# Performance work log

Hardware: AMD Instinct MI355X
Metric: run time of the kernel (lower is better)

The kernel has to match this reference:

```python
import jax, jax.numpy as jnp
import numpy as np

NUM_HEADS = 16
HEAD_DIM = 64
ROT_DIM = HEAD_DIM // 2  # RotaryEmbedding(dim=head_dim/2) rotates first 32 dims only
THETA = 10000.0


def _rope(x):
    # x: [b, h, l, d]; interleaved (lucidrains) rotary on first ROT_DIM dims.
    L = x.shape[-2]
    inv_freq = 1.0 / (THETA ** (jnp.arange(0, ROT_DIM, 2, dtype=jnp.float32) / ROT_DIM))  # [ROT_DIM/2]
    ang = jnp.arange(L, dtype=jnp.float32)[:, None] * inv_freq[None, :]  # [l, ROT_DIM/2]
    ang = jnp.repeat(ang, 2, axis=-1)  # [l, ROT_DIM] (each freq repeated for the pair)
    cos, sin = jnp.cos(ang), jnp.sin(ang)
    x_rot, x_pass = x[..., :ROT_DIM], x[..., ROT_DIM:]
    x1 = x_rot[..., 0::2]
    x2 = x_rot[..., 1::2]
    rot_half = jnp.stack([-x2, x1], axis=-1).reshape(x_rot.shape)  # rotate_half, interleaved
    x_rot = x_rot * cos + rot_half * sin
    return jnp.concatenate([x_rot, x_pass], axis=-1)


def setup_inputs() -> dict:
    key = jax.random.key(0)
    ks = jax.random.split(key, 7)
    B, L, E = 2, 2048, 1024
    s = 1.0 / np.sqrt(E)
    return {
        "query": jax.random.normal(ks[0], (B, L, E), jnp.float32),
        "key": jax.random.normal(ks[1], (B, L, E), jnp.float32),
        "value": jax.random.normal(ks[2], (B, L, E), jnp.float32),
        "Wq": jax.random.normal(ks[3], (E, E), jnp.float32) * s,
        "Wk": jax.random.normal(ks[4], (E, E), jnp.float32) * s,
        "Wv": jax.random.normal(ks[5], (E, E), jnp.float32) * s,
        "Wo": jax.random.normal(ks[6], (E, E), jnp.float32) * s,
        "bo": jnp.zeros((E,), jnp.float32),
    }


def reference(query, key, value, Wq, Wk, Wv, Wo, bo):
    B, L, E = query.shape
    H, D = NUM_HEADS, HEAD_DIM
    scaling = D ** (-0.5)

    def split_heads(x):
        return x.reshape(B, L, H, D).transpose(0, 2, 1, 3)  # b h l d

    q = split_heads(query @ Wq.T)
    k = split_heads(key @ Wk.T)
    v = split_heads(value @ Wv.T)
    q = _rope(q)
    k = _rope(k)
    # NOTE: source divides by scaling (multiplies by sqrt(D)) -- faithful to original.
    attn_weight = jnp.einsum('bhid,bhjd->bhij', q, k) / scaling
    # NOTE: softmax over dim=-2 (query axis), as in the original code.
    attn_weight = jax.nn.softmax(attn_weight, axis=-2)
    attn = jnp.einsum('bhij,bhjd->bhid', attn_weight, v)
    attn = attn.transpose(0, 2, 1, 3).reshape(B, L, E)
    out = attn @ Wo.T + bo
    return out, attn_weight
```

## Files before the change

### kernel.cpp

```cpp
#include <hip/hip_runtime.h>
#include <cmath>

typedef __bf16 bf16;
typedef __attribute__((ext_vector_type(4))) __bf16 bf16x4;
typedef __attribute__((ext_vector_type(8))) __bf16 bf16x8;
typedef __attribute__((ext_vector_type(4))) float f32x4;

#define MFMA16(a, b, c) __builtin_amdgcn_mfma_f32_16x16x32_bf16((a), (b), (c), 0, 0, 0)
#define SETPRIO1 __builtin_amdgcn_s_setprio(1)
#define SETPRIO0 __builtin_amdgcn_s_setprio(0)
#define EXP2(x) __builtin_amdgcn_exp2f(x)
#define WAITV_BAR(N) asm volatile("s_waitcnt vmcnt(" #N ")\n\ts_barrier" ::: "memory")
#define WAITL_BAR    asm volatile("s_waitcnt lgkmcnt(0)\n\ts_barrier" ::: "memory")

#define LOG2E 1.4426950408889634f

static __device__ __forceinline__ void gload16(const bf16* g, bf16* l)
{
  __builtin_amdgcn_global_load_lds((const __attribute__((address_space(1))) void*)g,
                                   (__attribute__((address_space(3))) void*)l, 16, 0, 0);
}

static __device__ __forceinline__ void split4(const float4 v, bf16x4& h, bf16x4& l)
{
  h[0] = (bf16)v.x; l[0] = (bf16)(v.x - (float)h[0]);
  h[1] = (bf16)v.y; l[1] = (bf16)(v.y - (float)h[1]);
  h[2] = (bf16)v.z; l[2] = (bf16)(v.z - (float)h[2]);
  h[3] = (bf16)v.w; l[3] = (bf16)(v.w - (float)h[3]);
}

__global__ __launch_bounds__(256) void conv_kernel(
    const float* __restrict__ query, const float* __restrict__ key, const float* __restrict__ value,
    const float* __restrict__ Wq, const float* __restrict__ Wk, const float* __restrict__ Wv,
    const float* __restrict__ Wo,
    bf16* __restrict__ qh, bf16* __restrict__ ql, bf16* __restrict__ kh, bf16* __restrict__ kl,
    bf16* __restrict__ wqh, bf16* __restrict__ wql, bf16* __restrict__ wkh, bf16* __restrict__ wkl,
    bf16* __restrict__ vb, bf16* __restrict__ wvb, bf16* __restrict__ wob)
{
  const int i = blockIdx.x * 256 + threadIdx.x;
  const float* src;
  bf16 *dh, *dl;
  int e;
  if (i < 1048576)      { src = query; dh = qh; dl = ql; e = i; }
  else if (i < 2097152) { src = key;   dh = kh; dl = kl; e = i - 1048576; }
  else if (i < 3145728) { src = value; dh = vb; dl = nullptr; e = i - 2097152; }
  else {
    const int w = i - 3145728;
    const int which = w >> 18;
    e = w & 262143;
    src = (which == 0) ? Wq : (which == 1) ? Wk : (which == 2) ? Wv : Wo;
    dh  = (which == 0) ? wqh : (which == 1) ? wkh : (which == 2) ? wvb : wob;
    dl  = (which == 0) ? wql : (which == 1) ? wkl : nullptr;
  }
  const float4 v = ((const float4*)src)[e];
  bf16x4 h, l;
  split4(v, h, l);
  *(bf16x4*)(dh + (size_t)e * 4) = h;
  if (dl) *(bf16x4*)(dl + (size_t)e * 4) = l;
}

__global__ __launch_bounds__(256) void projqk_kernel(
    const bf16* __restrict__ qh, const bf16* __restrict__ ql,
    const bf16* __restrict__ kh, const bf16* __restrict__ kl,
    const bf16* __restrict__ wqh, const bf16* __restrict__ wql,
    const bf16* __restrict__ wkh, const bf16* __restrict__ wkl,
    bf16* __restrict__ Qh_g, bf16* __restrict__ Ql_g,
    bf16* __restrict__ Kh_g, bf16* __restrict__ Kl_g)
{
  const int which = blockIdx.y;
  const bf16* ta[4];
  ta[0] = which ? kh : qh;   ta[1] = which ? kl : ql;
  ta[2] = which ? wkh : wqh; ta[3] = which ? wkl : wql;
  bf16* oh = which ? Kh_g : Qh_g;
  bf16* ol = which ? Kl_g : Ql_g;
  const float oscale = which ? 8.0f * LOG2E : 1.0f;

  __shared__ __align__(16) bf16 sm[2][4][4096];
  const int tid = threadIdx.x, lane = tid & 63, w = tid >> 6;
  const int wm = w >> 1, wn = w & 1;
  const int fr = lane & 15, fg = lane >> 4;
  const int bm = blockIdx.x >> 3, bn = blockIdx.x & 7;
  const int rb[4] = {bm * 128, bm * 128, bn * 128, bn * 128};
  const int lrow = lane >> 2, lcol = (lane & 3) * 8;

  auto stage = [&](int buf, int kt) {
#pragma unroll
    for (int tl = 0; tl < 4; ++tl)
#pragma unroll
      for (int q = 0; q < 2; ++q) {
        const int r = (q * 4 + w) * 16 + lrow;
        gload16(ta[tl] + (size_t)(rb[tl] + r) * 1024 + kt * 32 + lcol,
                &sm[buf][tl][(q * 4 + w) * 512]);
      }
  };

  f32x4 acc[4][4] = {};
  stage(0, 0);
  for (int kt = 0; kt < 32; ++kt) {
    const int cur = kt & 1;
    if (kt < 31) { stage(cur ^ 1, kt + 1); WAITV_BAR(8); }
    else         { WAITV_BAR(0); }
    bf16x8 afh[4], afl[4], bfh[4], bfl[4];
#pragma unroll
    for (int m = 0; m < 4; ++m) {
      afh[m] = *(bf16x8*)&sm[cur][0][(wm * 64 + m * 16 + fr) * 32 + fg * 8];
      afl[m] = *(bf16x8*)&sm[cur][1][(wm * 64 + m * 16 + fr) * 32 + fg * 8];
    }
#pragma unroll
    for (int n = 0; n < 4; ++n) {
      bfh[n] = *(bf16x8*)&sm[cur][2][(wn * 64 + n * 16 + fr) * 32 + fg * 8];
      bfl[n] = *(bf16x8*)&sm[cur][3][(wn * 64 + n * 16 + fr) * 32 + fg * 8];
    }
    SETPRIO1;
#pragma unroll
    for (int m = 0; m < 4; ++m)
#pragma unroll
      for (int n = 0; n < 4; ++n) {
        acc[m][n] = MFMA16(afh[m], bfh[n], acc[m][n]);
        acc[m][n] = MFMA16(afh[m], bfl[n], acc[m][n]);
        acc[m][n] = MFMA16(afl[m], bfh[n], acc[m][n]);
      }
    SETPRIO0;
    WAITL_BAR;
  }
#pragma unroll
  for (int n = 0; n < 4; ++n) {
    const int d = n * 16 + fr;
    const bool rot = (n < 2);
    const float invf = rot ? exp2f((float)(d >> 1) * (-0.83048202372184059f)) : 0.0f;
    const int odd = d & 1;
    const int col = bn * 128 + wn * 64 + n * 16 + fr;
#pragma unroll
    for (int m = 0; m < 4; ++m)
#pragma unroll
      for (int r4 = 0; r4 < 4; ++r4) {
        const int row = bm * 128 + wm * 64 + m * 16 + fg * 4 + r4;
        float x = acc[m][n][r4];
        const float p = __shfl_xor(x, 1);
        if (rot) {
          float sn, cs;
          sincosf((float)(row & 2047) * invf, &sn, &cs);
          x = odd ? x * cs + p * sn : x * cs - p * sn;
        }
        x *= oscale;
        const bf16 hv = (bf16)x;
        oh[(size_t)row * 1024 + col] = hv;
        ol[(size_t)row * 1024 + col] = (bf16)(x - (float)hv);
      }
  }
}

__global__ __launch_bounds__(256) void projv_kernel(const bf16* __restrict__ vb,
                                                    const bf16* __restrict__ wvb,
                                                    bf16* __restrict__ Vt_g)
{
  __shared__ __align__(16) bf16 sm[2][2][4096];
  const int tid = threadIdx.x, lane = tid & 63, w = tid >> 6;
  const int wm = w >> 1, wn = w & 1;
  const int fr = lane & 15, fg = lane >> 4;
  const int bm = blockIdx.x >> 3, bn = blockIdx.x & 7;
  const int lrow = lane >> 2, lcol = (lane & 3) * 8;

  auto stage = [&](int buf, int kt) {
#pragma unroll
    for (int q = 0; q < 2; ++q) {
      const int r = (q * 4 + w) * 16 + lrow;
      gload16(vb  + (size_t)(bm * 128 + r) * 1024 + kt * 32 + lcol, &sm[buf][0][(q * 4 + w) * 512]);
      gload16(wvb + (size_t)(bn * 128 + r) * 1024 + kt * 32 + lcol, &sm[buf][1][(q * 4 + w) * 512]);
    }
  };

  f32x4 acc[4][4] = {};
  stage(0, 0);
  for (int kt = 0; kt < 32; ++kt) {
    const int cur = kt & 1;
    if (kt < 31) { stage(cur ^ 1, kt + 1); WAITV_BAR(4); }
    else         { WAITV_BAR(0); }
    bf16x8 af[4], bf[4];
#pragma unroll
    for (int m = 0; m < 4; ++m) af[m] = *(bf16x8*)&sm[cur][0][(wm * 64 + m * 16 + fr) * 32 + fg * 8];
#pragma unroll
    for (int n = 0; n < 4; ++n) bf[n] = *(bf16x8*)&sm[cur][1][(wn * 64 + n * 16 + fr) * 32 + fg * 8];
    SETPRIO1;
#pragma unroll
    for (int m = 0; m < 4; ++m)
#pragma unroll
      for (int n = 0; n < 4; ++n) acc[m][n] = MFMA16(af[m], bf[n], acc[m][n]);
    SETPRIO0;
    WAITL_BAR;
  }
#pragma unroll
  for (int m = 0; m < 4; ++m) {
    const int row0 = bm * 128 + wm * 64 + m * 16 + fg * 4;
    const int b = row0 >> 11, l0 = row0 & 2047;
#pragma unroll
    for (int n = 0; n < 4; ++n) {
      const int col = bn * 128 + wn * 64 + n * 16 + fr;
      const int h = col >> 6, d = col & 63;
      bf16x4 pk;
#pragma unroll
      for (int j = 0; j < 4; ++j) pk[j] = (bf16)acc[m][n][j];
      *(bf16x4*)(Vt_g + ((size_t)((b * 16 + h) * 64 + d)) * 2048 + l0) = pk;
    }
  }
}

__global__ __launch_bounds__(256) void out_kernel(const bf16* __restrict__ attnb,
                                                  const bf16* __restrict__ wob,
                                                  const float* __restrict__ bo,
                                                  float* __restrict__ out)
{
  __shared__ __align__(16) bf16 sm[2][2][4096];
  const int tid = threadIdx.x, lane = tid & 63, w = tid >> 6;
  const int wm = w >> 1, wn = w & 1;
  const int fr = lane & 15, fg = lane >> 4;
  const int bm = blockIdx.x >> 3, bn = blockIdx.x & 7;
  const int lrow = lane >> 2, lcol = (lane & 3) * 8;

  auto stage = [&](int buf, int kt) {
#pragma unroll
    for (int q = 0; q < 2; ++q) {
      const int r = (q * 4 + w) * 16 + lrow;
      gload16(attnb + (size_t)(bm * 128 + r) * 1024 + kt * 32 + lcol, &sm[buf][0][(q * 4 + w) * 512]);
      gload16(wob   + (size_t)(bn * 128 + r) * 1024 + kt * 32 + lcol, &sm[buf][1][(q * 4 + w) * 512]);
    }
  };

  f32x4 acc[4][4] = {};
  stage(0, 0);
  for (int kt = 0; kt < 32; ++kt) {
    const int cur = kt & 1;
    if (kt < 31) { stage(cur ^ 1, kt + 1); WAITV_BAR(4); }
    else         { WAITV_BAR(0); }
    bf16x8 af[4], bf[4];
#pragma unroll
    for (int m = 0; m < 4; ++m) af[m] = *(bf16x8*)&sm[cur][0][(wm * 64 + m * 16 + fr) * 32 + fg * 8];
#pragma unroll
    for (int n = 0; n < 4; ++n) bf[n] = *(bf16x8*)&sm[cur][1][(wn * 64 + n * 16 + fr) * 32 + fg * 8];
    SETPRIO1;
#pragma unroll
    for (int m = 0; m < 4; ++m)
#pragma unroll
      for (int n = 0; n < 4; ++n) acc[m][n] = MFMA16(af[m], bf[n], acc[m][n]);
    SETPRIO0;
    WAITL_BAR;
  }
#pragma unroll
  for (int m = 0; m < 4; ++m)
#pragma unroll
    for (int n = 0; n < 4; ++n) {
      const int col = bn * 128 + wn * 64 + n * 16 + fr;
      const float bv = bo[col];
#pragma unroll
      for (int r4 = 0; r4 < 4; ++r4) {
        const int row = bm * 128 + wm * 64 + m * 16 + fg * 4 + r4;
        out[(size_t)row * 1024 + col] = acc[m][n][r4] + bv;
      }
    }
}

__global__ __launch_bounds__(512) void stats_kernel(const bf16* __restrict__ Qh_g, const bf16* __restrict__ Ql_g,
                                                    const bf16* __restrict__ Kh_g, const bf16* __restrict__ Kl_g,
                                                    float* __restrict__ colmax, float* __restrict__ csuminv)
{
  __shared__ __align__(16) bf16 smh[2][8192], sml[2][8192];
  const int swz = (blockIdx.x & 7) * 64 + (blockIdx.x >> 3);
  const int bh = swz >> 4, jb = swz & 15;
  const int b = bh >> 4, h = bh & 15;
  const int t = threadIdx.x, lane = t & 63, w = t >> 6;
  const int fr = lane & 15, fg = lane >> 4;
  const int lr = lane >> 3, lc = lane & 7;

  auto stageQ = [&](int buf, int it) {
#pragma unroll
    for (int q = 0; q < 2; ++q) {
      const int r = (q * 8 + w) * 8 + lr;
      const size_t g = (size_t)(b * 2048 + it * 128 + r) * 1024 + h * 64 + ((lc ^ (r & 7)) * 8);
      gload16(Qh_g + g, &smh[buf][(q * 8 + w) * 512]);
      gload16(Ql_g + g, &sml[buf][(q * 8 + w) * 512]);
    }
  };

#pragma unroll
  for (int q = 0; q < 2; ++q) {
    const int r = (q * 8 + w) * 8 + lr;
    const size_t g = (size_t)(b * 2048 + jb * 128 + r) * 1024 + h * 64 + ((lc ^ (r & 7)) * 8);
    gload16(Kh_g + g, &smh[1][(q * 8 + w) * 512]);
    gload16(Kl_g + g, &sml[1][(q * 8 + w) * 512]);
  }
  stageQ(0, 0);
  WAITV_BAR(4);
  bf16x8 kfh[2], kfl[2];
#pragma unroll
  for (int ks = 0; ks < 2; ++ks) {
    const int rr = w * 16 + fr;
    const int cc = (ks * 32 + fg * 8) ^ ((rr & 7) << 3);
    kfh[ks] = *(bf16x8*)&smh[1][rr * 64 + cc];
    kfl[ks] = *(bf16x8*)&sml[1][rr * 64 + cc];
  }
  WAITL_BAR;

  float rm[4] = {-1e30f, -1e30f, -1e30f, -1e30f};
  float rs[4] = {0.f, 0.f, 0.f, 0.f};
  for (int it = 0; it < 16; ++it) {
    const int cur = it & 1;
    if (it < 15) { stageQ(cur ^ 1, it + 1); WAITV_BAR(4); }
    else         { WAITV_BAR(0); }
    f32x4 acc[8] = {};
    SETPRIO1;
#pragma unroll
    for (int ks = 0; ks < 2; ++ks)
#pragma unroll
      for (int n = 0; n < 8; ++n) {
        const int rr = n * 16 + fr;
        const int cc = (ks * 32 + fg * 8) ^ ((rr & 7) << 3);
        const bf16x8 qf = *(bf16x8*)&smh[cur][rr * 64 + cc];
        const bf16x8 lf = *(bf16x8*)&sml[cur][rr * 64 + cc];
        acc[n] = MFMA16(kfh[ks], qf, acc[n]);
        acc[n] = MFMA16(kfh[ks], lf, acc[n]);
        acc[n] = MFMA16(kfl[ks], qf, acc[n]);
      }
    SETPRIO0;
    float tm[4];
#pragma unroll
    for (int r4 = 0; r4 < 4; ++r4) {
      float m = acc[0][r4];
#pragma unroll
      for (int n = 1; n < 8; ++n) m = fmaxf(m, acc[n][r4]);
      tm[r4] = m;
    }
#pragma unroll
    for (int off = 1; off < 16; off <<= 1)
#pragma unroll
      for (int r4 = 0; r4 < 4; ++r4) tm[r4] = fmaxf(tm[r4], __shfl_xor(tm[r4], off));
#pragma unroll
    for (int r4 = 0; r4 < 4; ++r4) {
      const float mn = fmaxf(rm[r4], tm[r4]);
      float ts = 0.f;
#pragma unroll
      for (int n = 0; n < 8; ++n) ts += EXP2(acc[n][r4] - mn);
#pragma unroll
      for (int off = 1; off < 16; off <<= 1) ts += __shfl_xor(ts, off);
      rs[r4] = rs[r4] * EXP2(rm[r4] - mn) + ts;
      rm[r4] = mn;
    }
    WAITL_BAR;
  }
  if (fr == 0) {
#pragma unroll
    for (int r4 = 0; r4 < 4; ++r4) {
      const int j = jb * 128 + w * 16 + fg * 4 + r4;
      colmax[bh * 2048 + j] = rm[r4];
      csuminv[bh * 2048 + j] = 1.0f / rs[r4];
    }
  }
}

__global__ __launch_bounds__(256) void attn_kernel(const bf16* __restrict__ Qh_g, const bf16* __restrict__ Ql_g,
                                                   const bf16* __restrict__ Kh_g, const bf16* __restrict__ Kl_g,
                                                   const bf16* __restrict__ Vt_g,
                                                   const float* __restrict__ colmax, const float* __restrict__ csuminv,
                                                   float* __restrict__ P, bf16* __restrict__ attnb)
{
  __shared__ __align__(16) unsigned char smem[46080];
  bf16(*Kh)[72] = (bf16(*)[72])smem;
  bf16(*Kl)[72] = (bf16(*)[72])(smem + 9216);
  bf16(*Vt)[72] = (bf16(*)[72])(smem + 18432);
  bf16(*Pb)[72] = (bf16(*)[72])(smem + 27648);
  bf16(*Qh)[72] = (bf16(*)[72])smem;
  bf16(*Ql)[72] = (bf16(*)[72])(smem + 18432);

  const int swz = (blockIdx.x & 7) * 64 + (blockIdx.x >> 3);
  const int bh = swz >> 4, ib = swz & 15;
  const int b = bh >> 4, h = bh & 15;
  const int t = threadIdx.x, lane = t & 63, w = t >> 6;
  const int fr = lane & 15, fg = lane >> 4;

#pragma unroll
  for (int q = 0; q < 4; ++q) {
    const int u = q * 256 + t, r = u >> 3, c8 = (u & 7) * 8;
    const size_t g = (size_t)(b * 2048 + ib * 128 + r) * 1024 + h * 64 + c8;
    *(bf16x8*)&Qh[r][c8] = *(const bf16x8*)(Qh_g + g);
    *(bf16x8*)&Ql[r][c8] = *(const bf16x8*)(Ql_g + g);
  }
  WAITL_BAR;
  bf16x8 qfh[2][2], qfl[2][2];
#pragma unroll
  for (int mf = 0; mf < 2; ++mf)
#pragma unroll
    for (int ks = 0; ks < 2; ++ks) {
      qfh[mf][ks] = *(bf16x8*)&Qh[w * 32 + mf * 16 + fr][ks * 32 + fg * 8];
      qfl[mf][ks] = *(bf16x8*)&Ql[w * 32 + mf * 16 + fr][ks * 32 + fg * 8];
    }

  bf16x8 rKh[2], rKl[2], rV[2];
  auto loadT = [&](int jt1) {
#pragma unroll
    for (int q = 0; q < 2; ++q) {
      const int u = q * 256 + t, r = u >> 3, c8 = (u & 7) * 8;
      const size_t g = (size_t)(b * 2048 + jt1 * 64 + r) * 1024 + h * 64 + c8;
      rKh[q] = *(const bf16x8*)(Kh_g + g);
      rKl[q] = *(const bf16x8*)(Kl_g + g);
      rV[q]  = *(const bf16x8*)(Vt_g + (size_t)(bh * 64 + r) * 2048 + jt1 * 64 + c8);
    }
  };
  auto writeT = [&]() {
#pragma unroll
    for (int q = 0; q < 2; ++q) {
      const int u = q * 256 + t, r = u >> 3, c8 = (u & 7) * 8;
      *(bf16x8*)&Kh[r][c8] = rKh[q];
      *(bf16x8*)&Kl[r][c8] = rKl[q];
      *(bf16x8*)&Vt[r][c8] = rV[q];
    }
  };

  loadT(0);
  WAITL_BAR;
  writeT();
  WAITL_BAR;

  f32x4 oacc[2][4] = {};
  for (int jt = 0; jt < 32; ++jt) {
    if (jt < 31) loadT(jt + 1);
    f32x4 s[2][4] = {};
    SETPRIO1;
#pragma unroll
    for (int ks = 0; ks < 2; ++ks)
#pragma unroll
      for (int nj = 0; nj < 4; ++nj) {
        const bf16x8 khf = *(bf16x8*)&Kh[nj * 16 + fr][ks * 32 + fg * 8];
        const bf16x8 klf = *(bf16x8*)&Kl[nj * 16 + fr][ks * 32 + fg * 8];
#pragma unroll
        for (int mf = 0; mf < 2; ++mf) {
          s[mf][nj] = MFMA16(qfh[mf][ks], khf, s[mf][nj]);
          s[mf][nj] = MFMA16(qfh[mf][ks], klf, s[mf][nj]);
          s[mf][nj] = MFMA16(qfl[mf][ks], khf, s[mf][nj]);
        }
      }
    SETPRIO0;
#pragma unroll
    for (int nj = 0; nj < 4; ++nj) {
      const int jg = jt * 64 + nj * 16 + fr;
      const float cm = colmax[bh * 2048 + jg];
      const float rcs = csuminv[bh * 2048 + jg];
#pragma unroll
      for (int mf = 0; mf < 2; ++mf)
#pragma unroll
        for (int r4 = 0; r4 < 4; ++r4) {
          const int il = w * 32 + mf * 16 + fg * 4 + r4;
          const float pv = EXP2(s[mf][nj][r4] - cm) * rcs;
          P[(size_t)(bh * 2048 + ib * 128 + il) * 2048 + jg] = pv;
          Pb[il][nj * 16 + fr] = (bf16)pv;
        }
    }
    WAITL_BAR;
    SETPRIO1;
#pragma unroll
    for (int ks = 0; ks < 2; ++ks) {
      bf16x8 pa[2];
#pragma unroll
      for (int mf = 0; mf < 2; ++mf) pa[mf] = *(bf16x8*)&Pb[w * 32 + mf * 16 + fr][ks * 32 + fg * 8];
#pragma unroll
      for (int nd = 0; nd < 4; ++nd) {
        const bf16x8 vbf = *(bf16x8*)&Vt[nd * 16 + fr][ks * 32 + fg * 8];
#pragma unroll
        for (int mf = 0; mf < 2; ++mf) oacc[mf][nd] = MFMA16(pa[mf], vbf, oacc[mf][nd]);
      }
    }
    SETPRIO0;
    WAITL_BAR;
    if (jt < 31) { writeT(); WAITL_BAR; }
  }
#pragma unroll
  for (int mf = 0; mf < 2; ++mf)
#pragma unroll
    for (int nd = 0; nd < 4; ++nd)
#pragma unroll
      for (int r4 = 0; r4 < 4; ++r4) {
        const int il = ib * 128 + w * 32 + mf * 16 + fg * 4 + r4;
        attnb[(size_t)(b * 2048 + il) * 1024 + h * 64 + nd * 16 + fr] = (bf16)oacc[mf][nd][r4];
      }
}

extern "C" void kernel_launch(void* const* d_in, const int* in_sizes, int n_in,
                              void* d_out, int out_size, void* d_ws, size_t ws_size,
                              hipStream_t stream)
{
  const float* query = (const float*)d_in[0];
  const float* key   = (const float*)d_in[1];
  const float* value = (const float*)d_in[2];
  const float* Wq    = (const float*)d_in[3];
  const float* Wk    = (const float*)d_in[4];
  const float* Wv    = (const float*)d_in[5];
  const float* Wo    = (const float*)d_in[6];
  const float* bo    = (const float*)d_in[7];

  float* out = (float*)d_out;
  float* P   = out + 4194304;

  bf16* qh  = (bf16*)(P + 0);
  bf16* ql  = (bf16*)(P + 2097152);
  bf16* kh  = (bf16*)(P + 4194304);
  bf16* kl  = (bf16*)(P + 6291456);
  bf16* wqh = (bf16*)(P + 8388608);
  bf16* wql = (bf16*)(P + 8912896);
  bf16* wkh = (bf16*)(P + 9437184);
  bf16* wkl = (bf16*)(P + 9961472);
  bf16* vb  = (bf16*)(P + 10485760);
  bf16* wvb = (bf16*)(P + 12582912);

  float* ws   = (float*)d_ws;
  bf16* Qh_g  = (bf16*)(ws + 0);
  bf16* Ql_g  = (bf16*)(ws + 2097152);
  bf16* Kh_g  = (bf16*)(ws + 4194304);
  bf16* Kl_g  = (bf16*)(ws + 6291456);
  bf16* Vt_g  = (bf16*)(ws + 8388608);
  bf16* attnb = (bf16*)(ws + 10485760);
  bf16* wob   = (bf16*)(ws + 12582912);
  float* cmax = ws + 13107200;
  float* csui = ws + 13172736;

  conv_kernel<<<16384, 256, 0, stream>>>(query, key, value, Wq, Wk, Wv, Wo,
                                         qh, ql, kh, kl, wqh, wql, wkh, wkl, vb, wvb, wob);
  projqk_kernel<<<dim3(256, 2), 256, 0, stream>>>(qh, ql, kh, kl, wqh, wql, wkh, wkl,
                                                  Qh_g, Ql_g, Kh_g, Kl_g);
  projv_kernel<<<256, 256, 0, stream>>>(vb, wvb, Vt_g);
  stats_kernel<<<512, 512, 0, stream>>>(Qh_g, Ql_g, Kh_g, Kl_g, cmax, csui);
  attn_kernel<<<512, 256, 0, stream>>>(Qh_g, Ql_g, Kh_g, Kl_g, Vt_g, cmax, csui, P, attnb);
  out_kernel<<<256, 256, 0, stream>>>(attnb, wob, bo, out);
}
```

Measured before the change: 373.4 us.

## Defer softmax stat reductions to end and split K/V smem writes to drop a barrier

The column-stats kernel now keeps per-lane running max and sum and does the cross-lane shuffle reduction once after the loop, with rescaling, instead of every iteration. In the attention kernel, colmax/csuminv loads are hoisted before the QK MFMAs so their latency overlaps compute. The K tile is written to LDS right after the P barrier, while the V write is deferred to after the PV barrier, which removes one barrier per iteration. The K write relies on QK reads having finished at the Pb barrier, and the V write relies on the next iteration's barrier for visibility.

```diff
diff --git a/kernel.cpp b/kernel.cpp
--- a/kernel.cpp
+++ b/kernel.cpp
@@ -321,30 +321,29 @@
         acc[n] = MFMA16(kfl[ks], qf, acc[n]);
       }
     SETPRIO0;
-    float tm[4];
 #pragma unroll
     for (int r4 = 0; r4 < 4; ++r4) {
-      float m = acc[0][r4];
-#pragma unroll
-      for (int n = 1; n < 8; ++n) m = fmaxf(m, acc[n][r4]);
-      tm[r4] = m;
-    }
-#pragma unroll
-    for (int off = 1; off < 16; off <<= 1)
-#pragma unroll
-      for (int r4 = 0; r4 < 4; ++r4) tm[r4] = fmaxf(tm[r4], __shfl_xor(tm[r4], off));
-#pragma unroll
-    for (int r4 = 0; r4 < 4; ++r4) {
-      const float mn = fmaxf(rm[r4], tm[r4]);
+      const float m = fmaxf(fmaxf(fmaxf(acc[0][r4], acc[1][r4]), fmaxf(acc[2][r4], acc[3][r4])),
+                            fmaxf(fmaxf(acc[4][r4], acc[5][r4]), fmaxf(acc[6][r4], acc[7][r4])));
+      const float mn = fmaxf(rm[r4], m);
       float ts = 0.f;
 #pragma unroll
       for (int n = 0; n < 8; ++n) ts += EXP2(acc[n][r4] - mn);
-#pragma unroll
-      for (int off = 1; off < 16; off <<= 1) ts += __shfl_xor(ts, off);
       rs[r4] = rs[r4] * EXP2(rm[r4] - mn) + ts;
       rm[r4] = mn;
     }
     WAITL_BAR;
+  }
+#pragma unroll
+  for (int r4 = 0; r4 < 4; ++r4) {
+    float M = rm[r4];
+#pragma unroll
+    for (int off = 1; off < 16; off <<= 1) M = fmaxf(M, __shfl_xor(M, off));
+    float s = rs[r4] * EXP2(rm[r4] - M);
+#pragma unroll
+    for (int off = 1; off < 16; off <<= 1) s += __shfl_xor(s, off);
+    rm[r4] = M;
+    rs[r4] = s;
   }
   if (fr == 0) {
 #pragma unroll
@@ -404,24 +403,37 @@
       rV[q]  = *(const bf16x8*)(Vt_g + (size_t)(bh * 64 + r) * 2048 + jt1 * 64 + c8);
     }
   };
-  auto writeT = [&]() {
+  auto writeK = [&]() {
 #pragma unroll
     for (int q = 0; q < 2; ++q) {
       const int u = q * 256 + t, r = u >> 3, c8 = (u & 7) * 8;
       *(bf16x8*)&Kh[r][c8] = rKh[q];
       *(bf16x8*)&Kl[r][c8] = rKl[q];
+    }
+  };
+  auto writeV = [&]() {
+#pragma unroll
+    for (int q = 0; q < 2; ++q) {
+      const int u = q * 256 + t, r = u >> 3, c8 = (u & 7) * 8;
       *(bf16x8*)&Vt[r][c8] = rV[q];
     }
   };
 
   loadT(0);
   WAITL_BAR;
-  writeT();
+  writeK(); writeV();
   WAITL_BAR;
 
   f32x4 oacc[2][4] = {};
   for (int jt = 0; jt < 32; ++jt) {
     if (jt < 31) loadT(jt + 1);
+    float cmr[4], rcr[4];
+#pragma unroll
+    for (int nj = 0; nj < 4; ++nj) {
+      const int jg = jt * 64 + nj * 16 + fr;
+      cmr[nj] = colmax[bh * 2048 + jg];
+      rcr[nj] = csuminv[bh * 2048 + jg];
+    }
     f32x4 s[2][4] = {};
     SETPRIO1;
 #pragma unroll
@@ -441,19 +453,18 @@
 #pragma unroll
     for (int nj = 0; nj < 4; ++nj) {
       const int jg = jt * 64 + nj * 16 + fr;
-      const float cm = colmax[bh * 2048 + jg];
-      const float rcs = csuminv[bh * 2048 + jg];
 #pragma unroll
       for (int mf = 0; mf < 2; ++mf)
 #pragma unroll
         for (int r4 = 0; r4 < 4; ++r4) {
           const int il = w * 32 + mf * 16 + fg * 4 + r4;
-          const float pv = EXP2(s[mf][nj][r4] - cm) * rcs;
+          const float pv = EXP2(s[mf][nj][r4] - cmr[nj]) * rcr[nj];
           P[(size_t)(bh * 2048 + ib * 128 + il) * 2048 + jg] = pv;
           Pb[il][nj * 16 + fr] = (bf16)pv;
         }
     }
     WAITL_BAR;
+    if (jt < 31) writeK();
     SETPRIO1;
 #pragma unroll
     for (int ks = 0; ks < 2; ++ks) {
@@ -469,7 +480,7 @@
     }
     SETPRIO0;
     WAITL_BAR;
-    if (jt < 31) { writeT(); WAITL_BAR; }
+    if (jt < 31) writeV();
   }
 #pragma unroll
   for (int mf = 0; mf < 2; ++mf)
```

New measurement: 367.3 us. Within noise of the previous version (-1.6%).
